# Performance work log

Measured on AMD Instinct MI355X. Metric: run time of the kernel, lower is better.

## Reference

```python
import jax, jax.numpy as jnp
import numpy as np

B, C, IMG, P = 32, 3, 224, 16
D, H, L, F, NCLS = 768, 12, 12, 3072, 1000
NP = (IMG // P) ** 2  # 196
DH = D // H  # 64
EPS = 1e-5


def _ln(x, g, b):
    m = jnp.mean(x, axis=-1, keepdims=True)
    v = jnp.mean(jnp.square(x - m), axis=-1, keepdims=True)
    return (x - m) * jax.lax.rsqrt(v + EPS) * g + b


def setup_inputs() -> dict:
    key = jax.random.key(0)
    ks = iter(jax.random.split(key, 32))
    s = 0.02
    rn = lambda shape: jax.random.normal(next(ks), shape, dtype=jnp.float32) * s
    inp = {
        "x": jax.random.normal(next(ks), (B, C, IMG, IMG), dtype=jnp.float32),
        "Wp": rn((P * P * C, D)), "bp": jnp.zeros((D,), jnp.float32),
        "cls": rn((1, 1, D)), "pos": rn((1, NP + 1, D)),
        # per-layer stacked params (leading dim L)
        "ln1_g": jnp.ones((L, D), jnp.float32), "ln1_b": jnp.zeros((L, D), jnp.float32),
        "Wq": rn((L, H, D, DH)), "bq": jnp.zeros((L, H, DH), jnp.float32),
        "Wk": rn((L, H, D, DH)), "bk": jnp.zeros((L, H, DH), jnp.float32),
        "Wv": rn((L, H, D, DH)), "bv": jnp.zeros((L, H, DH), jnp.float32),
        "Wo": rn((L, D, D)), "bo": jnp.zeros((L, D), jnp.float32),
        "ln2_g": jnp.ones((L, D), jnp.float32), "ln2_b": jnp.zeros((L, D), jnp.float32),
        "W1": rn((L, D, F)), "b1": jnp.zeros((L, F), jnp.float32),
        "W2": rn((L, F, D)), "b2": jnp.zeros((L, D), jnp.float32),
        # classification head
        "hln_g": jnp.ones((D,), jnp.float32), "hln_b": jnp.zeros((D,), jnp.float32),
        "hW1": rn((D, D)), "hb1": jnp.zeros((D,), jnp.float32),
        "hW2": rn((D, NCLS)), "hb2": jnp.zeros((NCLS,), jnp.float32),
    }
    return inp


def _vit(x, Wp, bp, cls, pos, ln1_g, ln1_b, Wq, bq, Wk, bk, Wv, bv, Wo, bo,
         ln2_g, ln2_b, W1, b1, W2, b2, hln_g, hln_b, hW1, hb1, hW2, hb2):
    b = x.shape[0]
    g = IMG // P
    # nn.Unfold(k=16, s=16): channel order (c, kh, kw), patch order (ph, pw)
    patches = x.reshape(b, C, g, P, g, P).transpose(0, 2, 4, 1, 3, 5).reshape(b, NP, C * P * P)
    h = patches @ Wp + bp  # [b, NP, D]
    h = jnp.concatenate([jnp.broadcast_to(cls, (b, 1, D)), h], axis=1) + pos  # [b, S, D]

    scale = 1.0 / jnp.sqrt(jnp.asarray(DH, h.dtype))

    def step(h, p):
        g1, b1_, wq, bq_, wk, bk_, wv, bv_, wo, bo_, g2, b2_, w1, bb1, w2, bb2 = p
        xn = _ln(h, g1, b1_)
        q = jnp.einsum('bsd,hde->bhse', xn, wq) + bq_[:, None, :]
        k = jnp.einsum('bsd,hde->bhse', xn, wk) + bk_[:, None, :]
        v = jnp.einsum('bsd,hde->bhse', xn, wv) + bv_[:, None, :]
        scores = jnp.einsum('bhse,bhte->bhst', q, k) * scale
        attn = jax.nn.softmax(scores, axis=-1)
        o = jnp.einsum('bhst,bhte->bhse', attn, v)  # [b,H,S,DH]
        o = o.transpose(0, 2, 1, 3).reshape(b, -1, D)  # concat heads
        h = o @ wo + bo_ + h
        xn = _ln(h, g2, b2_)
        h = jax.nn.gelu(xn @ w1 + bb1, approximate=False) @ w2 + bb2 + h
        return h, None

    params = (ln1_g, ln1_b, Wq, bq, Wk, bk, Wv, bv, Wo, bo, ln2_g, ln2_b, W1, b1, W2, b2)
    h, _ = jax.lax.scan(step, h, params)

    c = h[:, 0, :]
    c = _ln(c, hln_g, hln_b)
    return jax.nn.gelu(c @ hW1 + hb1, approximate=False) @ hW2 + hb2


def reference(x, Wp, bp, cls, pos, ln1_g, ln1_b, Wq, bq, Wk, bk, Wv, bv, Wo, bo,
              ln2_g, ln2_b, W1, b1, W2, b2, hln_g, hln_b, hW1, hb1, hW2, hb2):
    return _vit(x, Wp, bp, cls, pos, ln1_g, ln1_b, Wq, bq, Wk, bk, Wv, bv, Wo, bo,
                ln2_g, ln2_b, W1, b1, W2, b2, hln_g, hln_b, hW1, hb1, hW2, hb2)
```

## Files before the change

### kernel.cpp

```cpp
#include <hip/hip_runtime.h>

typedef unsigned short u16;
typedef __attribute__((ext_vector_type(8))) short short8;
typedef __attribute__((ext_vector_type(4))) float f32x4;

#define NTOK 6304
#define SP 197

#define OFF_WQKVT 0L
#define OFF_WOT   42467328L
#define OFF_W1T   56623104L
#define OFF_W2T   113246208L
#define OFF_WPT   169869312L
#define OFF_BQKV  171048960L
#define OFF_H     171159552L
#define OFF_XN    190525440L
#define OFF_QKV   200208384L
#define OFF_SC    229257216L
#define OFF_PM1   288867840L
#define OFF_VT    327599616L
#define OFF_CN    340182528L
#define OFF_T1    340280832L
#define WS_NEEDED 340379136L

__device__ __forceinline__ u16 f2bf(float x) {
  unsigned int u = __float_as_uint(x);
  u += 0x7fffu + ((u >> 16) & 1u);
  return (u16)(u >> 16);
}

__device__ __forceinline__ float gelu_f(float x) {
  return 0.5f * x * (1.0f + erff(x * 0.70710678118654752f));
}

__device__ __forceinline__ void gload_lds16(const void* g, void* l) {
  __builtin_amdgcn_global_load_lds(
      (const __attribute__((address_space(1))) unsigned int*)g,
      (__attribute__((address_space(3))) unsigned int*)l, 16, 0, 0);
}

template <bool BIAS, bool GELU, bool RES, bool OBF16, bool REMAP>
__global__ __launch_bounds__(512, 2) void gemm_w(
    const u16* __restrict__ A, int lda,
    const u16* __restrict__ Bm, int ldb,
    void* Cv, int ldc,
    const float* __restrict__ bias, const float* res, int ldres,
    int M, int N, int K, int tilesN) {
  __shared__ __align__(16) char smem[49152];

  const int t = threadIdx.x;
  const int l = t & 63;
  const int lr = l & 15, kb = (l >> 4) & 3;
  const int wid = t >> 6;
  const int wr = wid >> 1;
  const int wc = wid & 1;

  const int nwg = gridDim.x;
  const int orig = blockIdx.x;
  const int q8 = nwg >> 3, r8 = nwg & 7;
  const int xcd = orig & 7, loc = orig >> 3;
  const int wg =
      (xcd < r8 ? xcd * (q8 + 1) : r8 * (q8 + 1) + (xcd - r8) * q8) + loc;
  const int tn = wg % tilesN, tm = wg / tilesN;
  const int m0 = tm * 256, n0 = tn * 128;
  const int Mm1 = M - 1, Nm1 = N - 1;

  const f32x4 zf = {0.f, 0.f, 0.f, 0.f};
  f32x4 acc[4][4];
#pragma unroll
  for (int m = 0; m < 4; ++m)
#pragma unroll
    for (int n = 0; n < 4; ++n) acc[m][n] = zf;

  auto stage = [&](int k0) {
#pragma unroll
    for (int p = 0; p < 4; ++p) {
      int idx = p * 512 + t;
      int r = idx >> 3, cl = idx & 7;
      int cg = cl ^ (r & 7);
      int rr = m0 + r;
      rr = rr > Mm1 ? Mm1 : rr;
      gload_lds16(A + (long)rr * lda + k0 + cg * 8,
                  smem + ((p * 512 + (t & ~63)) << 4));
    }
#pragma unroll
    for (int p = 0; p < 2; ++p) {
      int idx = p * 512 + t;
      int r = idx >> 3, cl = idx & 7;
      int cg = cl ^ (r & 7);
      int rr = n0 + r;
      rr = rr > Nm1 ? Nm1 : rr;
      gload_lds16(Bm + (long)rr * ldb + k0 + cg * 8,
                  smem + 32768 + ((p * 512 + (t & ~63)) << 4));
    }
  };

  const int KT = K >> 6;
  for (int kt = 0; kt < KT; ++kt) {
    stage(kt * 64);
    __syncthreads();
    const char* Ab = smem;
    const char* Bb = smem + 32768;
#pragma unroll
    for (int kk = 0; kk < 2; ++kk) {
      const int ch = ((((kk << 2) | kb) ^ (lr & 7)) << 4);
      short8 af[4], bfv[4];
#pragma unroll
      for (int m = 0; m < 4; ++m)
        af[m] = *(const short8*)(Ab + (wr * 64 + m * 16 + lr) * 128 + ch);
#pragma unroll
      for (int n = 0; n < 4; ++n)
        bfv[n] = *(const short8*)(Bb + (wc * 64 + n * 16 + lr) * 128 + ch);
#pragma unroll
      for (int m = 0; m < 4; ++m)
#pragma unroll
        for (int n = 0; n < 4; ++n)
          acc[m][n] = __builtin_amdgcn_mfma_f32_16x16x32_bf16(af[m], bfv[n],
                                                              acc[m][n], 0, 0, 0);
    }
    __syncthreads();
  }

#pragma unroll
  for (int n = 0; n < 4; ++n) {
    const int gc = n0 + wc * 64 + n * 16 + lr;
    if (gc >= N) continue;
    const float bv = BIAS ? bias[gc] : 0.0f;
#pragma unroll
    for (int m = 0; m < 4; ++m) {
#pragma unroll
      for (int j = 0; j < 4; ++j) {
        const int gr = m0 + wr * 64 + m * 16 + kb * 4 + j;
        if (gr >= M) continue;
        float v = acc[m][n][j] + bv;
        if (RES) v += res[(long)gr * ldres + gc];
        if (GELU) v = gelu_f(v);
        long orow = gr;
        if (REMAP) orow = (long)(gr / 196) * 197 + (gr % 196) + 1;
        if (OBF16)
          ((u16*)Cv)[orow * (long)ldc + gc] = f2bf(v);
        else
          ((float*)Cv)[orow * (long)ldc + gc] = v;
      }
    }
  }
}

template <int BM, int BN, int WM, int WN, bool BIAS, bool GELU, bool RES,
          bool OBF16, bool REMAP>
__global__ __launch_bounds__(WM * WN * 64, 2) void gemm2(
    const u16* __restrict__ A, int lda,
    const u16* __restrict__ Bm, int ldb,
    void* Cv, int ldc,
    const float* __restrict__ bias, const float* res, int ldres,
    int M, int N, int K, int tilesN) {
  constexpr int THREADS = WM * WN * 64;
  constexpr int TM = BM / WM, TN = BN / WN;
  constexpr int FM = TM / 16, FN = TN / 16;
  constexpr int APT = (BM * 8) / THREADS;
  constexpr int BPT = (BN * 8) / THREADS;
  constexpr int ABYTES = BM * 128;
  constexpr int BUF = ABYTES + BN * 128;
  __shared__ __align__(16) char smem[2 * BUF];

  const int t = threadIdx.x;
  const int l = t & 63;
  const int lr = l & 15, kb = (l >> 4) & 3;
  const int wid = t >> 6;
  const int wr = wid / WN, wc = wid % WN;

  const int nwg = gridDim.x;
  const int orig = blockIdx.x;
  const int q8 = nwg >> 3, r8 = nwg & 7;
  const int xcd = orig & 7, loc = orig >> 3;
  const int wg =
      (xcd < r8 ? xcd * (q8 + 1) : r8 * (q8 + 1) + (xcd - r8) * q8) + loc;
  const int tn = wg % tilesN, tm = wg / tilesN;
  const int m0 = tm * BM, n0 = tn * BN;
  const int Mm1 = M - 1, Nm1 = N - 1;

  const f32x4 zf = {0.f, 0.f, 0.f, 0.f};
  f32x4 acc[FM][FN];
#pragma unroll
  for (int fm = 0; fm < FM; ++fm)
#pragma unroll
    for (int fn = 0; fn < FN; ++fn) acc[fm][fn] = zf;

  auto stage = [&](int kt, int d) {
    const int k0 = kt << 6;
    char* base = smem + d * BUF;
#pragma unroll
    for (int p = 0; p < APT; ++p) {
      int idx = p * THREADS + t;
      int r = idx >> 3, cl = idx & 7;
      int rr = m0 + r;
      rr = rr > Mm1 ? Mm1 : rr;
      gload_lds16(A + (long)rr * lda + k0 + ((cl ^ (r & 7)) << 3),
                  base + ((p * THREADS + (t & ~63)) << 4));
    }
    char* bbase = base + ABYTES;
#pragma unroll
    for (int p = 0; p < BPT; ++p) {
      int idx = p * THREADS + t;
      int r = idx >> 3, cl = idx & 7;
      int rr = n0 + r;
      rr = rr > Nm1 ? Nm1 : rr;
      gload_lds16(Bm + (long)rr * ldb + k0 + ((cl ^ (r & 7)) << 3),
                  bbase + ((p * THREADS + (t & ~63)) << 4));
    }
  };

  const int nt = K >> 6;
  stage(0, 0);
  __syncthreads();

  for (int kt = 0; kt < nt; ++kt) {
    if (kt + 1 < nt) stage(kt + 1, (kt + 1) & 1);
    const char* Ab = smem + (kt & 1) * BUF;
    const char* Bb = Ab + ABYTES;
#pragma unroll
    for (int kk = 0; kk < 2; ++kk) {
      const int ch = ((((kk << 2) | kb) ^ (lr & 7)) << 4);
      short8 af[FM], bf[FN];
#pragma unroll
      for (int fm = 0; fm < FM; ++fm)
        af[fm] = *(const short8*)(Ab + (wr * TM + fm * 16 + lr) * 128 + ch);
#pragma unroll
      for (int fn = 0; fn < FN; ++fn)
        bf[fn] = *(const short8*)(Bb + (wc * TN + fn * 16 + lr) * 128 + ch);
#pragma unroll
      for (int fm = 0; fm < FM; ++fm)
#pragma unroll
        for (int fn = 0; fn < FN; ++fn)
          acc[fm][fn] = __builtin_amdgcn_mfma_f32_16x16x32_bf16(af[fm], bf[fn],
                                                                acc[fm][fn], 0, 0, 0);
    }
    __syncthreads();
  }

#pragma unroll
  for (int fn = 0; fn < FN; ++fn) {
    const int gc = n0 + wc * TN + fn * 16 + lr;
    if (gc >= N) continue;
    const float bv = BIAS ? bias[gc] : 0.0f;
#pragma unroll
    for (int fm = 0; fm < FM; ++fm) {
#pragma unroll
      for (int j = 0; j < 4; ++j) {
        const int gr = m0 + wr * TM + fm * 16 + kb * 4 + j;
        if (gr >= M) continue;
        float v = acc[fm][fn][j] + bv;
        if (RES) v += res[(long)gr * ldres + gc];
        if (GELU) v = gelu_f(v);
        long orow = gr;
        if (REMAP) orow = (long)(gr / 196) * 197 + (gr % 196) + 1;
        if (OBF16)
          ((u16*)Cv)[orow * (long)ldc + gc] = f2bf(v);
        else
          ((float*)Cv)[orow * (long)ldc + gc] = v;
      }
    }
  }
}

__global__ __launch_bounds__(256) void k_attn(const u16* __restrict__ qkv,
                                              u16* __restrict__ o) {
  __shared__ __align__(16) u16 Kb[208 * 72];
  __shared__ __align__(16) u16 Vt[64 * 232];
  __shared__ __align__(16) u16 Pl[4][16 * 232];

  const int t = threadIdx.x;
  const int z = blockIdx.x;
  const int b = z / 12, hh = z % 12;
  const long qbase = (long)b * SP * 2304 + hh * 64;

#pragma unroll
  for (int p = 0; p < 7; ++p) {
    int idx = p * 256 + t;
    int row = idx >> 3, c = idx & 7;
    short8 kv = {0, 0, 0, 0, 0, 0, 0, 0};
    short8 vv = {0, 0, 0, 0, 0, 0, 0, 0};
    if (row < SP) {
      kv = *(const short8*)(qkv + qbase + 768 + (long)row * 2304 + c * 8);
      vv = *(const short8*)(qkv + qbase + 1536 + (long)row * 2304 + c * 8);
    }
    if (row < 208) *(short8*)(&Kb[row * 72 + c * 8]) = kv;
#pragma unroll
    for (int j = 0; j < 8; ++j) Vt[(c * 8 + j) * 232 + row] = ((const u16*)&vv)[j];
  }
  __syncthreads();

  const int l = t & 63, wid = t >> 6;
  const int lr = l & 15, kb = l >> 4;
  u16* Pw = Pl[wid];
  const f32x4 zf = {0.f, 0.f, 0.f, 0.f};

  for (int st = wid; st < 13; st += 4) {
    int qrow = st * 16 + lr;
    qrow = qrow > SP - 1 ? SP - 1 : qrow;
    short8 qf[2];
#pragma unroll
    for (int kk = 0; kk < 2; ++kk)
      qf[kk] = *(const short8*)(qkv + qbase + (long)qrow * 2304 + kk * 32 + kb * 8);

    f32x4 s[13];
#pragma unroll
    for (int nt = 0; nt < 13; ++nt) {
      s[nt] = zf;
#pragma unroll
      for (int kk = 0; kk < 2; ++kk) {
        short8 kf = *(const short8*)(&Kb[(nt * 16 + lr) * 72 + kk * 32 + kb * 8]);
        s[nt] = __builtin_amdgcn_mfma_f32_16x16x32_bf16(qf[kk], kf, s[nt], 0, 0, 0);
      }
    }

    float mx[4] = {-1e30f, -1e30f, -1e30f, -1e30f};
#pragma unroll
    for (int nt = 0; nt < 13; ++nt) {
      const bool pred = (nt < 12) | (lr < 5);
#pragma unroll
      for (int j = 0; j < 4; ++j) {
        float v = s[nt][j] * 0.125f;
        s[nt][j] = v;
        if (pred) mx[j] = fmaxf(mx[j], v);
      }
    }
#pragma unroll
    for (int o4 = 1; o4 < 16; o4 <<= 1)
#pragma unroll
      for (int j = 0; j < 4; ++j) mx[j] = fmaxf(mx[j], __shfl_xor(mx[j], o4));
    float sum[4] = {0.f, 0.f, 0.f, 0.f};
#pragma unroll
    for (int nt = 0; nt < 13; ++nt) {
      const bool pred = (nt < 12) | (lr < 5);
#pragma unroll
      for (int j = 0; j < 4; ++j) {
        float p = pred ? __expf(s[nt][j] - mx[j]) : 0.f;
        s[nt][j] = p;
        sum[j] += p;
      }
    }
#pragma unroll
    for (int o4 = 1; o4 < 16; o4 <<= 1)
#pragma unroll
      for (int j = 0; j < 4; ++j) sum[j] += __shfl_xor(sum[j], o4);
    float inv[4];
#pragma unroll
    for (int j = 0; j < 4; ++j) inv[j] = 1.0f / sum[j];

#pragma unroll
    for (int nt = 0; nt < 13; ++nt)
#pragma unroll
      for (int j = 0; j < 4; ++j)
        Pw[(kb * 4 + j) * 232 + nt * 16 + lr] = f2bf(s[nt][j] * inv[j]);
#pragma unroll
    for (int j = 0; j < 4; ++j) Pw[(kb * 4 + j) * 232 + 208 + lr] = 0;

    short8 pf[7];
#pragma unroll
    for (int kk = 0; kk < 7; ++kk)
      pf[kk] = *(const short8*)(&Pw[lr * 232 + kk * 32 + kb * 8]);
#pragma unroll
    for (int dt = 0; dt < 4; ++dt) {
      f32x4 oacc = zf;
#pragma unroll
      for (int kk = 0; kk < 7; ++kk) {
        short8 vf = *(const short8*)(&Vt[(dt * 16 + lr) * 232 + kk * 32 + kb * 8]);
        oacc = __builtin_amdgcn_mfma_f32_16x16x32_bf16(pf[kk], vf, oacc, 0, 0, 0);
      }
#pragma unroll
      for (int j = 0; j < 4; ++j) {
        int qr = st * 16 + kb * 4 + j;
        if (qr < SP)
          o[((long)b * SP + qr) * 768 + hh * 64 + dt * 16 + lr] = f2bf(oacc[j]);
      }
    }
  }
}

__global__ void k_wt64(const float* __restrict__ W, u16* __restrict__ out,
                       int sel) {
  __shared__ float tile[32][33];
  const int z = blockIdx.z;
  const int ly = z / 12, hh = z % 12;
  const float* ip = W + (long)z * 768 * 64;
  u16* op = out + (long)ly * 2304 * 768 + ((long)sel * 768 + hh * 64) * 768;
  const int c0 = blockIdx.x * 32, r0 = blockIdx.y * 32;
  const int tx = threadIdx.x, ty = threadIdx.y;
#pragma unroll
  for (int i = 0; i < 4; ++i)
    tile[ty + i * 8][tx] = ip[(long)(r0 + ty + i * 8) * 64 + c0 + tx];
  __syncthreads();
#pragma unroll
  for (int i = 0; i < 4; ++i)
    op[(long)(c0 + ty + i * 8) * 768 + r0 + tx] = f2bf(tile[tx][ty + i * 8]);
}

__global__ void k_bqkv(const float* __restrict__ bq, const float* __restrict__ bk,
                       const float* __restrict__ bv, float* __restrict__ out) {
  int idx = blockIdx.x * 256 + threadIdx.x;
  if (idx >= 27648) return;
  int c = idx % 2304, ly = idx / 2304;
  int sel = c / 768, cc = c % 768;
  const float* b = sel == 0 ? bq : (sel == 1 ? bk : bv);
  out[idx] = b[ly * 768 + cc];
}

__global__ void k_transpose(const float* __restrict__ in, u16* __restrict__ out,
                            int R, int C) {
  __shared__ float tile[32][33];
  long zoff = (long)blockIdx.z * R * C;
  const float* ip = in + zoff;
  u16* op = out + zoff;
  int c0 = blockIdx.x * 32, r0 = blockIdx.y * 32;
  int tx = threadIdx.x, ty = threadIdx.y;
#pragma unroll
  for (int i = 0; i < 4; ++i)
    tile[ty + i * 8][tx] = ip[(long)(r0 + ty + i * 8) * C + c0 + tx];
  __syncthreads();
#pragma unroll
  for (int i = 0; i < 4; ++i)
    op[(long)(c0 + ty + i * 8) * R + r0 + tx] = f2bf(tile[tx][ty + i * 8]);
}

__global__ void k_patchify(const float* __restrict__ x, u16* __restrict__ out) {
  long idx = (long)blockIdx.x * 256 + threadIdx.x;
  int f = (int)(idx % 768);
  long rp = idx / 768;
  int p = (int)(rp % 196), b = (int)(rp / 196);
  int gy = p / 14, gx = p % 14;
  int c = f >> 8, rem = f & 255;
  int i = rem >> 4, j = rem & 15;
  out[idx] = f2bf(x[(((long)b * 3 + c) * 224 + gy * 16 + i) * 224 + gx * 16 + j]);
}

__global__ void k_add_pos(float* h, const float* __restrict__ cls,
                          const float* __restrict__ pos) {
  long idx = (long)blockIdx.x * 256 + threadIdx.x;
  int d4 = (int)(idx % 192);
  long rs = idx / 192;
  int s = (int)(rs % 197);
  float4* hp = (float4*)h;
  const float4* pp = (const float4*)pos;
  if (s == 0) {
    const float4* cp = (const float4*)cls;
    float4 v = cp[d4], w = pp[d4];
    v.x += w.x; v.y += w.y; v.z += w.z; v.w += w.w;
    hp[idx] = v;
  } else {
    float4 v = hp[idx], w = pp[(long)s * 192 + d4];
    v.x += w.x; v.y += w.y; v.z += w.z; v.w += w.w;
    hp[idx] = v;
  }
}

__global__ __launch_bounds__(256) void k_ln(const float* __restrict__ in,
                                            const float* __restrict__ g,
                                            const float* __restrict__ b,
                                            u16* __restrict__ out, int rows) {
  int w = threadIdx.x >> 6, l = threadIdx.x & 63;
  int row = blockIdx.x * 4 + w;
  if (row >= rows) return;
  const float4* ip = (const float4*)(in + (long)row * 768);
  float4 v[3];
  float s = 0.f, sq = 0.f;
#pragma unroll
  for (int i = 0; i < 3; ++i) {
    v[i] = ip[i * 64 + l];
    s += v[i].x + v[i].y + v[i].z + v[i].w;
    sq += v[i].x * v[i].x + v[i].y * v[i].y + v[i].z * v[i].z + v[i].w * v[i].w;
  }
#pragma unroll
  for (int o = 1; o < 64; o <<= 1) {
    s += __shfl_xor(s, o);
    sq += __shfl_xor(sq, o);
  }
  const float m = s * (1.f / 768.f);
  const float rs = rsqrtf(sq * (1.f / 768.f) - m * m + 1e-5f);
  ushort4* op = (ushort4*)(out + (long)row * 768);
#pragma unroll
  for (int i = 0; i < 3; ++i) {
    int c4 = (i * 64 + l) * 4;
    float4 gv = *(const float4*)(g + c4);
    float4 bv = *(const float4*)(b + c4);
    ushort4 o4;
    o4.x = f2bf((v[i].x - m) * rs * gv.x + bv.x);
    o4.y = f2bf((v[i].y - m) * rs * gv.y + bv.y);
    o4.z = f2bf((v[i].z - m) * rs * gv.z + bv.z);
    o4.w = f2bf((v[i].w - m) * rs * gv.w + bv.w);
    op[i * 64 + l] = o4;
  }
}

__global__ void k_head_ln(const float* __restrict__ h, const float* __restrict__ g,
                          const float* __restrict__ b, float* __restrict__ out) {
  const int bb = blockIdx.x, l = threadIdx.x;
  const float4* ip = (const float4*)(h + (long)bb * 197 * 768);
  float4 v[3];
  float s = 0.f, sq = 0.f;
#pragma unroll
  for (int i = 0; i < 3; ++i) {
    v[i] = ip[i * 64 + l];
    s += v[i].x + v[i].y + v[i].z + v[i].w;
    sq += v[i].x * v[i].x + v[i].y * v[i].y + v[i].z * v[i].z + v[i].w * v[i].w;
  }
#pragma unroll
  for (int o = 1; o < 64; o <<= 1) {
    s += __shfl_xor(s, o);
    sq += __shfl_xor(sq, o);
  }
  const float m = s * (1.f / 768.f);
  const float rs = rsqrtf(sq * (1.f / 768.f) - m * m + 1e-5f);
  float4* op = (float4*)(out + bb * 768);
#pragma unroll
  for (int i = 0; i < 3; ++i) {
    int c4 = (i * 64 + l) * 4;
    float4 gv = *(const float4*)(g + c4);
    float4 bv = *(const float4*)(b + c4);
    float4 o4;
    o4.x = (v[i].x - m) * rs * gv.x + bv.x;
    o4.y = (v[i].y - m) * rs * gv.y + bv.y;
    o4.z = (v[i].z - m) * rs * gv.z + bv.z;
    o4.w = (v[i].w - m) * rs * gv.w + bv.w;
    op[i * 64 + l] = o4;
  }
}

template <bool GELU>
__global__ __launch_bounds__(256) void k_head_gemm(
    const float* __restrict__ in, const float* __restrict__ W,
    const float* __restrict__ bias, float* __restrict__ out, int K, int N) {
  __shared__ float partial[4][64];
  const int b = blockIdx.y;
  const int cl = threadIdx.x & 63;
  const int c = blockIdx.x * 64 + cl;
  const int kp = threadIdx.x >> 6;
  const int kc = K >> 2;
  float s = 0.f;
  if (c < N) {
    const float* ip = in + (long)b * K + kp * kc;
    const float* wp = W + (long)(kp * kc) * N + c;
    for (int k = 0; k < kc; ++k) s = fmaf(ip[k], wp[(long)k * N], s);
  }
  partial[kp][cl] = s;
  __syncthreads();
  if (kp == 0 && c < N) {
    float v = partial[0][cl] + partial[1][cl] + partial[2][cl] + partial[3][cl] +
              bias[c];
    if (GELU) v = gelu_f(v);
    out[(long)b * N + c] = v;
  }
}

extern "C" void kernel_launch(void* const* d_in, const int* in_sizes, int n_in,
                              void* d_out, int out_size, void* d_ws, size_t ws_size,
                              hipStream_t stream) {
  (void)in_sizes; (void)n_in; (void)out_size;
  if ((long)ws_size < WS_NEEDED) return;

  const float* x = (const float*)d_in[0];
  const float* Wp = (const float*)d_in[1];
  const float* bp = (const float*)d_in[2];
  const float* cls = (const float*)d_in[3];
  const float* pos = (const float*)d_in[4];
  const float* ln1g = (const float*)d_in[5];
  const float* ln1b = (const float*)d_in[6];
  const float* Wq = (const float*)d_in[7];
  const float* bq = (const float*)d_in[8];
  const float* Wk = (const float*)d_in[9];
  const float* bk = (const float*)d_in[10];
  const float* Wv = (const float*)d_in[11];
  const float* bv = (const float*)d_in[12];
  const float* Wo = (const float*)d_in[13];
  const float* bo = (const float*)d_in[14];
  const float* ln2g = (const float*)d_in[15];
  const float* ln2b = (const float*)d_in[16];
  const float* W1 = (const float*)d_in[17];
  const float* b1 = (const float*)d_in[18];
  const float* W2 = (const float*)d_in[19];
  const float* b2 = (const float*)d_in[20];
  const float* hlng = (const float*)d_in[21];
  const float* hlnb = (const float*)d_in[22];
  const float* hW1 = (const float*)d_in[23];
  const float* hb1 = (const float*)d_in[24];
  const float* hW2 = (const float*)d_in[25];
  const float* hb2 = (const float*)d_in[26];

  char* ws = (char*)d_ws;
  u16* wqkvt = (u16*)(ws + OFF_WQKVT);
  u16* wot = (u16*)(ws + OFF_WOT);
  u16* w1t = (u16*)(ws + OFF_W1T);
  u16* w2t = (u16*)(ws + OFF_W2T);
  u16* wpt = (u16*)(ws + OFF_WPT);
  float* bqkv = (float*)(ws + OFF_BQKV);
  float* h = (float*)(ws + OFF_H);
  u16* xn = (u16*)(ws + OFF_XN);
  u16* qkv = (u16*)(ws + OFF_QKV);
  u16* pbuf = qkv;
  u16* m1 = (u16*)(ws + OFF_PM1);
  float* cn = (float*)(ws + OFF_CN);
  float* t1 = (float*)(ws + OFF_T1);

  k_wt64<<<dim3(2, 24, 144), dim3(32, 8), 0, stream>>>(Wq, wqkvt, 0);
  k_wt64<<<dim3(2, 24, 144), dim3(32, 8), 0, stream>>>(Wk, wqkvt, 1);
  k_wt64<<<dim3(2, 24, 144), dim3(32, 8), 0, stream>>>(Wv, wqkvt, 2);
  k_bqkv<<<108, 256, 0, stream>>>(bq, bk, bv, bqkv);
  k_transpose<<<dim3(24, 24, 12), dim3(32, 8), 0, stream>>>(Wo, wot, 768, 768);
  k_transpose<<<dim3(96, 24, 12), dim3(32, 8), 0, stream>>>(W1, w1t, 768, 3072);
  k_transpose<<<dim3(24, 96, 12), dim3(32, 8), 0, stream>>>(W2, w2t, 3072, 768);
  k_transpose<<<dim3(24, 24, 1), dim3(32, 8), 0, stream>>>(Wp, wpt, 768, 768);

  k_patchify<<<18816, 256, 0, stream>>>(x, pbuf);
  gemm2<128, 128, 2, 2, true, false, false, false, true><<<294, 256, 0, stream>>>(
      pbuf, 768, wpt, 768, h, 768, bp, nullptr, 0, 6272, 768, 768, 6);
  k_add_pos<<<4728, 256, 0, stream>>>(h, cls, pos);

  for (int ly = 0; ly < 12; ++ly) {
    k_ln<<<1576, 256, 0, stream>>>(h, ln1g + ly * 768, ln1b + ly * 768, xn, NTOK);
    gemm_w<true, false, false, true, false><<<450, 512, 0, stream>>>(
        xn, 768, wqkvt + (long)ly * 2304 * 768, 768, qkv, 2304,
        bqkv + ly * 2304, nullptr, 0, NTOK, 2304, 768, 18);
    k_attn<<<384, 256, 0, stream>>>(qkv, xn);
    gemm2<128, 128, 2, 2, true, false, true, false, false><<<300, 256, 0, stream>>>(
        xn, 768, wot + (long)ly * 768 * 768, 768, h, 768,
        bo + ly * 768, h, 768, NTOK, 768, 768, 6);
    k_ln<<<1576, 256, 0, stream>>>(h, ln2g + ly * 768, ln2b + ly * 768, xn, NTOK);
    gemm_w<true, true, false, true, false><<<600, 512, 0, stream>>>(
        xn, 768, w1t + (long)ly * 3072 * 768, 768, m1, 3072,
        b1 + ly * 3072, nullptr, 0, NTOK, 3072, 768, 24);
    gemm2<128, 128, 2, 2, true, false, true, false, false><<<300, 256, 0, stream>>>(
        m1, 3072, w2t + (long)ly * 768 * 3072, 3072, h, 768,
        b2 + ly * 768, h, 768, NTOK, 768, 3072, 6);
  }

  k_head_ln<<<32, 64, 0, stream>>>(h, hlng, hlnb, cn);
  k_head_gemm<true><<<dim3(12, 32), 256, 0, stream>>>(cn, hW1, hb1, t1, 768, 768);
  k_head_gemm<false><<<dim3(16, 32), 256, 0, stream>>>(t1, hW2, hb2, (float*)d_out,
                                                       768, 1000);
}
```

Baseline: 3.285 ms.

## Use 128x128 single-buffered GEMM with XCD-aware tile remap for QKV projection

Adds a new 256-thread GEMM kernel with 128x128 tiles, K-step 64, XOR-swizzled LDS staging through global_load_lds, and a block-index remap that groups consecutive tiles on the same XCD. The QKV projection switches to it, going from 450 blocks of 512 threads to 900 blocks of 256. The aim is better occupancy (launch bounds allow 3 blocks per CU) and better L2 locality per XCD. In exchange it drops double buffering, so global loads are not overlapped with MFMA work.

```diff
diff --git a/kernel.cpp b/kernel.cpp
--- a/kernel.cpp
+++ b/kernel.cpp
@@ -37,6 +37,103 @@
   __builtin_amdgcn_global_load_lds(
       (const __attribute__((address_space(1))) unsigned int*)g,
       (__attribute__((address_space(3))) unsigned int*)l, 16, 0, 0);
+}
+
+template <bool BIAS, bool GELU, bool RES, bool OBF16, bool REMAP>
+__global__ __launch_bounds__(256, 3) void gemm_k(
+    const u16* __restrict__ A, int lda,
+    const u16* __restrict__ Bm, int ldb,
+    void* Cv, int ldc,
+    const float* __restrict__ bias, const float* res, int ldres,
+    int M, int N, int K, int tilesN) {
+  __shared__ float4 smemv[2048];
+  char* smem = (char*)smemv;
+
+  const int t = threadIdx.x;
+  const int nwg = gridDim.x;
+  const int orig = blockIdx.x;
+  const int q8 = nwg >> 3, r8 = nwg & 7;
+  const int xcd = orig & 7, loc = orig >> 3;
+  const int wg =
+      (xcd < r8 ? xcd * (q8 + 1) : r8 * (q8 + 1) + (xcd - r8) * q8) + loc;
+  const int tn = wg % tilesN, tm = wg / tilesN;
+  const int m0 = tm * 128, n0 = tn * 128;
+  const int l = t & 63;
+  const int lr = l & 15, kb = l >> 4;
+  const int wr = (t >> 7) & 1, wc = (t >> 6) & 1;
+
+  const f32x4 zf = {0.f, 0.f, 0.f, 0.f};
+  f32x4 acc[4][4];
+#pragma unroll
+  for (int m = 0; m < 4; ++m)
+#pragma unroll
+    for (int n = 0; n < 4; ++n) acc[m][n] = zf;
+
+  auto stage = [&](const u16* src, int ld, int row0, int maxrow, int k0,
+                   char* ldsbase) {
+#pragma unroll
+    for (int p = 0; p < 4; ++p) {
+      int idx = p * 256 + t;
+      int r = idx >> 3;
+      int cl = idx & 7;
+      int cg = cl ^ (r & 7);
+      int rr = row0 + r;
+      rr = rr > maxrow ? maxrow : rr;
+      gload_lds16(src + (long)rr * ld + k0 + cg * 8,
+                  ldsbase + (long)(p * 256 + (t & ~63)) * 16);
+    }
+  };
+
+  const int KT = K >> 6;
+  for (int kt = 0; kt < KT; ++kt) {
+    stage(A, lda, m0, M - 1, kt * 64, smem);
+    stage(Bm, ldb, n0, N - 1, kt * 64, smem + 16384);
+    __syncthreads();
+    const char* Ab = smem;
+    const char* Bb = smem + 16384;
+#pragma unroll
+    for (int kk = 0; kk < 2; ++kk) {
+      const int cla = ((kk << 2) + kb) ^ (lr & 7);
+      short8 af[4], bfv[4];
+#pragma unroll
+      for (int m = 0; m < 4; ++m)
+        af[m] = *(const short8*)(Ab + ((wr * 64 + m * 16 + lr) * 128 + cla * 16));
+#pragma unroll
+      for (int n = 0; n < 4; ++n)
+        bfv[n] = *(const short8*)(Bb + ((wc * 64 + n * 16 + lr) * 128 + cla * 16));
+#pragma unroll
+      for (int m = 0; m < 4; ++m)
+#pragma unroll
+        for (int n = 0; n < 4; ++n)
+          acc[m][n] = __builtin_amdgcn_mfma_f32_16x16x32_bf16(af[m], bfv[n],
+                                                              acc[m][n], 0, 0, 0);
+    }
+    __syncthreads();
+  }
+
+#pragma unroll
+  for (int n = 0; n < 4; ++n) {
+    const int gc = n0 + wc * 64 + n * 16 + lr;
+    if (gc >= N) continue;
+    const float bv = BIAS ? bias[gc] : 0.0f;
+#pragma unroll
+    for (int m = 0; m < 4; ++m) {
+#pragma unroll
+      for (int j = 0; j < 4; ++j) {
+        const int gr = m0 + wr * 64 + m * 16 + kb * 4 + j;
+        if (gr >= M) continue;
+        float v = acc[m][n][j] + bv;
+        if (RES) v += res[(long)gr * ldres + gc];
+        if (GELU) v = gelu_f(v);
+        long orow = gr;
+        if (REMAP) orow = (long)(gr / 196) * 197 + (gr % 196) + 1;
+        if (OBF16)
+          ((u16*)Cv)[orow * (long)ldc + gc] = f2bf(v);
+        else
+          ((float*)Cv)[orow * (long)ldc + gc] = v;
+      }
+    }
+  }
 }
 
 template <bool BIAS, bool GELU, bool RES, bool OBF16, bool REMAP>
@@ -617,7 +714,7 @@
 
   for (int ly = 0; ly < 12; ++ly) {
     k_ln<<<1576, 256, 0, stream>>>(h, ln1g + ly * 768, ln1b + ly * 768, xn, NTOK);
-    gemm_w<true, false, false, true, false><<<450, 512, 0, stream>>>(
+    gemm_k<true, false, false, true, false><<<900, 256, 0, stream>>>(
         xn, 768, wqkvt + (long)ly * 2304 * 768, 768, qkv, 2304,
         bqkv + ly * 2304, nullptr, 0, NTOK, 2304, 768, 18);
     k_attn<<<384, 256, 0, stream>>>(qkv, xn);
```

New measurement: 3.289 ms. About the same (+0.1%).
